# Kernel optimization log

Hardware: AMD Instinct MI355X
Metric: run time of the kernel (lower is better)

## Reference

```python
import jax, jax.numpy as jnp
import numpy as np

B, N, F, C, K = 8, 256, 64, 16, 2  # batch, agents, hidden_nf, hidden_c (coord channels), category_num
EPS = 1e-4


def _lin(x, W, b=None):
    y = jnp.einsum('...i,oi->...o', x, W)
    return y if b is None else y + b


def _forward(h, coord, vel, category, W_cv, W_e1, b_e1, W_e2, b_e2,
             W_cat1, b_cat1, W_cat2, b_cat2, W_f1, b_f1, W_f2, b_f2,
             W_n1, b_n1, W_n2, b_n2, W_ql, W_kl, W_qm, b_qm):
    relu = jax.nn.relu
    B_, N_, F_ = h.shape
    # --- edge model: dense pairwise features ---
    coord_diff = coord[:, :, None] - coord[:, None]            # [B,N,N,C,3]
    coord_dist = jnp.linalg.norm(coord_diff, axis=-1)          # [B,N,N,C]
    h1 = jnp.broadcast_to(h[:, :, None, :], (B_, N_, N_, F_))
    h2 = jnp.broadcast_to(h[:, None, :, :], (B_, N_, N_, F_))
    edge_h = jnp.concatenate([h1, h2, coord_dist], axis=-1)    # [B,N,N,2F+C]
    edge_feat = relu(_lin(relu(_lin(edge_h, W_e1, b_e1)), W_e2, b_e2))  # [B,N,N,F]
    # --- inner agent attention ---
    att = relu(_lin(h, W_qm, b_qm))[..., None]                 # [B,N,C,1]
    v = coord - jnp.mean(coord, axis=(1, 2), keepdims=True)
    coord = att * v + coord
    # --- reasoning-based coordinate aggregation (loop over K=2 categories) ---
    factors = jnp.zeros(edge_h.shape[:3] + (C,), coord.dtype)
    for i in range(K):
        ci = relu(_lin(relu(_lin(edge_h, W_cat1[i], b_cat1[i])), W_cat2[i], b_cat2[i]))
        factors = factors + category[..., i:i + 1] * ci
    factors = relu(_lin(relu(_lin(factors, W_f1, b_f1)), W_f2, b_f2))   # [B,N,N,C]
    coord = coord + jnp.sum(factors[..., None] * coord_diff, axis=2)    # [B,N,C,3]
    # --- velocity term (linear over channel dim) ---
    coord = coord + jnp.einsum('bncd,oc->bnod', vel, W_cv)
    # --- non-linear equivariant update ---
    cm = jnp.mean(coord, axis=(1, 2), keepdims=True)
    c = coord - cm
    q = jnp.einsum('bncd,oc->bnod', c, W_ql)
    k = jnp.einsum('bncd,oc->bnod', c, W_kl)
    prod = jnp.sum(q * k, axis=-1, keepdims=True)              # [B,N,C,1]
    mask = (prod >= 0).astype(c.dtype)
    kns = jnp.sum(k * k, axis=-1, keepdims=True)
    coord = mask * q + (1 - mask) * (q - prod / (kns + EPS) * k) + cm
    # --- node model: masked sum over neighbors (no self-edge) ---
    nb_mask = 1.0 - jnp.eye(N_, dtype=edge_feat.dtype)
    agg = jnp.einsum('bnmf,nm->bnf', edge_feat, nb_mask)
    h_out = h + _lin(relu(_lin(jnp.concatenate([h, agg], axis=-1), W_n1, b_n1)), W_n2, b_n2)
    return h_out, coord


def setup_inputs() -> dict:
    key = jax.random.key(0)
    ks = jax.random.split(key, 20)
    p = lambda i, shape, fan: jax.random.normal(ks[i], shape, jnp.float32) / np.sqrt(fan)
    z = lambda shape: jnp.zeros(shape, jnp.float32)
    return {
        'h': jax.random.normal(ks[0], (B, N, F), jnp.float32),
        'coord': jax.random.normal(ks[1], (B, N, C, 3), jnp.float32),
        'vel': jax.random.normal(ks[2], (B, N, C, 3), jnp.float32),
        'category': jax.random.uniform(ks[3], (B, N, N, K), jnp.float32),
        'W_cv': p(4, (C, C), C),
        'W_e1': p(5, (F, 2 * F + C), 2 * F + C), 'b_e1': z((F,)),
        'W_e2': p(6, (F, F), F), 'b_e2': z((F,)),
        'W_cat1': p(7, (K, F, 2 * F + C), 2 * F + C), 'b_cat1': z((K, F)),
        'W_cat2': p(8, (K, C, F), F), 'b_cat2': z((K, C)),
        'W_f1': p(9, (C, C), C), 'b_f1': z((C,)),
        'W_f2': p(10, (C, C), C), 'b_f2': z((C,)),
        'W_n1': p(11, (F, 2 * F), 2 * F), 'b_n1': z((F,)),
        'W_n2': p(12, (F, F), F), 'b_n2': z((F,)),
        'W_ql': p(13, (C, C), C),
        'W_kl': p(14, (C, C), C),
        'W_qm': p(15, (C, F), F), 'b_qm': z((C,)),
    }


def reference(h, coord, vel, category, W_cv, W_e1, b_e1, W_e2, b_e2,
              W_cat1, b_cat1, W_cat2, b_cat2, W_f1, b_f1, W_f2, b_f2,
              W_n1, b_n1, W_n2, b_n2, W_ql, W_kl, W_qm, b_qm):
    h_out, coord_out = _forward(h, coord, vel, category, W_cv, W_e1, b_e1, W_e2, b_e2,
                                W_cat1, b_cat1, W_cat2, b_cat2, W_f1, b_f1, W_f2, b_f2,
                                W_n1, b_n1, W_n2, b_n2, W_ql, W_kl, W_qm, b_qm)
    return (h_out, coord_out, category)
```

## Files before the change

kernel.cpp:

```cpp
#include <hip/hip_runtime.h>

typedef unsigned short u16;
typedef unsigned int u32;
typedef _Float16 f16;
typedef __attribute__((ext_vector_type(2))) _Float16 f16x2;
typedef __attribute__((ext_vector_type(4))) _Float16 f16x4;
typedef __attribute__((ext_vector_type(4))) float f32x4;

#define EPSV 1e-4f


static constexpr int WS_FLAG = 0;
static constexpr int WS_ATT  = 16;
static constexpr int WS_CT   = 32784;
static constexpr int WS_AGG  = 131088;
static constexpr int WS_CAC  = 262160;
static constexpr int WS_GWN1 = 360464;
static constexpr int WS_GWN2 = 364560;
static constexpr int WS_BN1  = 372752;
static constexpr int WS_BN2  = 372816;
static constexpr int WS_BIAS = 372880;
static constexpr int WS_GWD  = 373008;
static constexpr int WS_GWE2 = 374544;
static constexpr int WS_GWC2 = 376592;
static constexpr int WS_GWF1 = 377616;
static constexpr int WS_GWF2 = 377744;

static __device__ __forceinline__ float bfld(u16 v) {
  return __uint_as_float(((unsigned)v) << 16);
}
static __device__ __forceinline__ u16 f2b(float x) {
  unsigned u = __float_as_uint(x);
  u += 0x7FFFu + ((u >> 16) & 1u);
  return (u16)(u >> 16);
}
static __device__ __forceinline__ float ldv(const void* p, int i, int flag) {
  return flag ? bfld(((const u16*)p)[i]) : ((const float*)p)[i];
}
static __device__ __forceinline__ void stv(void* p, int i, float v, int flag) {
  if (flag) ((u16*)p)[i] = f2b(v);
  else      ((float*)p)[i] = v;
}
static __device__ __forceinline__ f16* scratchHA(void* outv, int flag) {
  return (f16*)((char*)outv + (size_t)229376 * (flag ? 2 : 4));
}
static __device__ __forceinline__ int sniff_flag(const void* h) {
  const u16* hu = (const u16*)h;
  int cnt = 0;
  for (int i = 0; i < 128; ++i) {
    unsigned e = (hu[i] >> 7) & 0xFFu;
    if ((e >= 100u && e <= 150u) || hu[i] == 0) ++cnt;
  }
  return (cnt >= 112) ? 1 : 0;
}
static __device__ __forceinline__ f16x4 pack4(float a, float b, float c, float d) {
  const f16x2 lo = __builtin_bit_cast(f16x2, __builtin_amdgcn_cvt_pkrtz(a, b));
  const f16x2 hi = __builtin_bit_cast(f16x2, __builtin_amdgcn_cvt_pkrtz(c, d));
  f16x4 r; r[0] = lo[0]; r[1] = lo[1]; r[2] = hi[0]; r[3] = hi[1]; return r;
}
static __device__ __forceinline__ f16x4 pack4_relu(float a, float b, float c, float d) {
  f16x2 lo = __builtin_bit_cast(f16x2, __builtin_amdgcn_cvt_pkrtz(a, b));
  f16x2 hi = __builtin_bit_cast(f16x2, __builtin_amdgcn_cvt_pkrtz(c, d));
  const f16x2 z = {(_Float16)0.f, (_Float16)0.f};
  lo = __builtin_elementwise_max(lo, z);
  hi = __builtin_elementwise_max(hi, z);
  f16x4 r; r[0] = lo[0]; r[1] = lo[1]; r[2] = hi[0]; r[3] = hi[1]; return r;
}
static __device__ __forceinline__ void st8h(f16* dst, uint4 v) {
  uint2 lo; lo.x = v.x; lo.y = v.y;
  uint2 hi; hi.x = v.z; hi.y = v.w;
  *(uint2*)dst = lo;
  *(uint2*)(dst + 4) = hi;
}
static __device__ __forceinline__ void load48(const void* p, int node, int flag,
                                              float* dst) {
  if (flag) {
    const uint4* q4 = (const uint4*)((const u16*)p + node * 48);
#pragma unroll
    for (int c = 0; c < 6; ++c) {
      const uint4 v = q4[c];
      const u32 a[4] = {v.x, v.y, v.z, v.w};
#pragma unroll
      for (int e = 0; e < 4; ++e) {
        dst[c * 8 + e * 2]     = bfld((u16)(a[e] & 0xFFFFu));
        dst[c * 8 + e * 2 + 1] = bfld((u16)(a[e] >> 16));
      }
    }
  } else {
    const float4* q4 = (const float4*)((const float*)p + node * 48);
#pragma unroll
    for (int c = 0; c < 12; ++c) {
      const float4 v = q4[c];
      dst[c * 4] = v.x; dst[c * 4 + 1] = v.y; dst[c * 4 + 2] = v.z; dst[c * 4 + 3] = v.w;
    }
  }
}
static __device__ __forceinline__ void stage_h64(const void* h, int hbase, int flag,
                                                 f16* sH, int tid) {
  if (flag) {
    const uint4* src = (const uint4*)((const u16*)h + hbase);
    for (int v = tid; v < 512; v += 256) {
      const uint4 x = src[v];
      const int e = v * 8;
      f16* dst = &sH[(e >> 6) * 68 + (e & 63)];
      const u32 a[4] = {x.x, x.y, x.z, x.w};
#pragma unroll
      for (int p = 0; p < 4; ++p) {
        dst[p * 2]     = (f16)bfld((u16)(a[p] & 0xFFFFu));
        dst[p * 2 + 1] = (f16)bfld((u16)(a[p] >> 16));
      }
    }
  } else {
    const float4* src = (const float4*)((const float*)h + hbase);
    for (int v = tid; v < 1024; v += 256) {
      const float4 x = src[v];
      const int e = v * 4;
      f16* dst = &sH[(e >> 6) * 68 + (e & 63)];
      dst[0] = (f16)x.x; dst[1] = (f16)x.y; dst[2] = (f16)x.z; dst[3] = (f16)x.w;
    }
  }
}

__global__ __launch_bounds__(256) void k_front(
    const void* __restrict__ h, const void* __restrict__ coord,
    const void* __restrict__ We1, const void* __restrict__ Wc1,
    const void* __restrict__ We2, const void* __restrict__ Wc2,
    const void* __restrict__ Wf1, const void* __restrict__ Wf2,
    const void* __restrict__ Wn1, const void* __restrict__ Wn2,
    const void* __restrict__ Wqm,
    const void* __restrict__ be1, const void* __restrict__ bc1,
    const void* __restrict__ bqm, const void* __restrict__ be2,
    const void* __restrict__ bc2, const void* __restrict__ bf1,
    const void* __restrict__ bf2, const void* __restrict__ bn1,
    const void* __restrict__ bn2,
    float* __restrict__ ws, void* __restrict__ outv) {
  const int blk = blockIdx.x, tid = threadIdx.x;
  __shared__ int sflag;
  if (tid == 0) {
    sflag = sniff_flag(h);
    if (blk == 0) ((int*)ws)[WS_FLAG] = sflag;
  }
  __syncthreads();
  const int flag = sflag;

  if (blk < 256) {
    const int t = blk * 256 + tid;
    const int STR = 65536;
    for (int idx = t; idx < 98304; idx += STR) {
      const int node = idx / 48, cd = idx - node * 48;
      ws[WS_CT + ((node >> 8) * 48 + cd) * 256 + (node & 255)] = ldv(coord, idx, flag);
    }
    f16* gwd  = (f16*)(ws + WS_GWD);
    f16* gwe2 = (f16*)(ws + WS_GWE2);
    f16* gwc2 = (f16*)(ws + WS_GWC2);
    f16* gwf1 = (f16*)(ws + WS_GWF1);
    f16* gwf2 = (f16*)(ws + WS_GWF2);
    for (int idx = t; idx < 3072; idx += STR) {
      const int o = idx >> 4, c = idx & 15;
      const void* src = (o < 64) ? We1 : Wc1;
      const int row = (o < 64) ? o : (o - 64);
      gwd[idx] = (f16)ldv(src, row * 144 + 128 + c, flag);
    }
    for (int idx = t; idx < 4096; idx += STR) gwe2[idx] = (f16)ldv(We2, idx, flag);
    for (int idx = t; idx < 2048; idx += STR) gwc2[idx] = (f16)ldv(Wc2, idx, flag);
    if (t < 256) { gwf1[t] = (f16)ldv(Wf1, t, flag); gwf2[t] = (f16)ldv(Wf2, t, flag); }
    f16* gwn1 = (f16*)(ws + WS_GWN1);
    f16* gwn2 = (f16*)(ws + WS_GWN2);
    for (int idx = t; idx < 8192; idx += STR) gwn1[idx] = (f16)ldv(Wn1, idx, flag);
    for (int idx = t; idx < 4096; idx += STR) gwn2[idx] = (f16)ldv(Wn2, idx, flag);
    if (t < 64)  ws[WS_BN1 + t] = ldv(bn1, t, flag);
    if (t >= 64 && t < 128) ws[WS_BN2 + t - 64] = ldv(bn2, t - 64, flag);
    if (t >= 128 && t < 192) ws[WS_BIAS + t - 128] = ldv(be2, t - 128, flag);
    if (t >= 192 && t < 224) ws[WS_BIAS + 64 + t - 192] = ldv(bc2, t - 192, flag);
    if (t >= 224 && t < 240) ws[WS_BIAS + 96 + t - 224] = ldv(bf1, t - 224, flag);
    if (t >= 240 && t < 256) ws[WS_BIAS + 112 + t - 240] = ldv(bf2, t - 240, flag);
    return;
  }

  const int gb = blk - 256;
  const int nt = gb / 5, grp = gb % 5;
  const int w = tid >> 6, lane = tid & 63;
  const int q = lane >> 4, l15 = lane & 15;
  f16* HA16 = scratchHA(outv, flag);
  f16* HBJ  = HA16 + 2048 * 192;
  __shared__ __align__(16) f16 sW[80 * 68];
  __shared__ __align__(16) f16 sH[64 * 68];
  __shared__ float sBias[80];
  if (flag) {
    for (int idx = tid; idx < 640; idx += 256) {
      const int r = idx >> 3, seg = idx & 7;
      const int row = grp * 80 + r;
      const u16* src;
      if (row < 64)       src = (const u16*)We1 + row * 144;
      else if (row < 192) src = (const u16*)Wc1 + (row - 64) * 144;
      else if (row < 384) {
        const int ro = row - 192;
        src = (ro < 64) ? (const u16*)We1 + ro * 144 + 64
                        : (const u16*)Wc1 + (ro - 64) * 144 + 64;
      } else              src = (const u16*)Wqm + (row - 384) * 64;
      const uint4 v = ((const uint4*)src)[seg];
      const u32 a[4] = {v.x, v.y, v.z, v.w};
      f16* dst = &sW[r * 68 + seg * 8];
#pragma unroll
      for (int p = 0; p < 4; ++p) {
        dst[p * 2]     = (f16)bfld((u16)(a[p] & 0xFFFFu));
        dst[p * 2 + 1] = (f16)bfld((u16)(a[p] >> 16));
      }
    }
  } else {
    for (int idx = tid; idx < 1280; idx += 256) {
      const int r = idx >> 4, seg = idx & 15;
      const int row = grp * 80 + r;
      const float* src;
      if (row < 64)       src = (const float*)We1 + row * 144;
      else if (row < 192) src = (const float*)Wc1 + (row - 64) * 144;
      else if (row < 384) {
        const int ro = row - 192;
        src = (ro < 64) ? (const float*)We1 + ro * 144 + 64
                        : (const float*)Wc1 + (ro - 64) * 144 + 64;
      } else              src = (const float*)Wqm + (row - 384) * 64;
      const float4 v = ((const float4*)src)[seg];
      f16x4 t; t[0] = (f16)v.x; t[1] = (f16)v.y; t[2] = (f16)v.z; t[3] = (f16)v.w;
      *(f16x4*)&sW[r * 68 + seg * 4] = t;
    }
  }
  stage_h64(h, nt * 64 * 64, flag, sH, tid);
  if (tid < 80) {
    const int row = grp * 80 + tid;
    sBias[tid] = (row < 64) ? ldv(be1, row, flag)
               : (row < 192) ? ldv(bc1, row - 64, flag)
               : (row < 384) ? 0.f : ldv(bqm, row - 384, flag);
  }
  __syncthreads();
  f16x4 Af[4];
#pragma unroll
  for (int ks = 0; ks < 4; ++ks)
    Af[ks] = *(const f16x4*)&sH[(w * 16 + l15) * 68 + ks * 16 + q * 4];
#pragma unroll
  for (int ot = 0; ot < 5; ++ot) {
    const float bv = sBias[ot * 16 + l15];
    f32x4 acc = (f32x4){bv, bv, bv, bv};
#pragma unroll
    for (int ks = 0; ks < 4; ++ks) {
      const f16x4 Bf = *(const f16x4*)&sW[(ot * 16 + l15) * 68 + ks * 16 + q * 4];
      acc = __builtin_amdgcn_mfma_f32_16x16x16f16(Af[ks], Bf, acc, 0, 0, 0);
    }
    const int out = grp * 80 + ot * 16 + l15;
    const int nodeD = nt * 64 + w * 16 + q * 4;
#pragma unroll
    for (int r = 0; r < 4; ++r) {
      const int node = nodeD + r;
      if (out < 192) {
        HA16[node * 192 + out] = (f16)acc[r];
      } else if (out < 384) {
        const int ol = out - 192;
        HBJ[(((node >> 8) * 48 + ((ol >> 4) << 2) + ((ol & 15) >> 2)) * 256 +
             (node & 255)) * 4 + (ol & 3)] = (f16)acc[r];
      } else {
        ws[WS_ATT + node * 16 + out - 384] = fmaxf(acc[r], 0.f);
      }
    }
  }
}

__global__ __launch_bounds__(256, 4) void k_edge(const void* __restrict__ cat,
                                                 float* __restrict__ ws,
                                                 void* __restrict__ outv) {
  const int node = ((blockIdx.x & 7) << 8) | (blockIdx.x >> 3);
  const int b = node >> 8, i = node & 255;
  const int tid = threadIdx.x;
  const int w = tid >> 6, lane = tid & 63, q = lane >> 4, l15 = lane & 15;
  const int flag = ((const int*)ws)[WS_FLAG];
  const f16* HA16 = scratchHA(outv, flag);
  const f16* HBJ  = HA16 + 2048 * 192;
  const float* __restrict__ cTb = ws + WS_CT + b * 48 * 256;

  __shared__ __align__(16) f16 sWd[192 * 20];
  __shared__ __align__(16) f16 sWe2[64 * 76];
  __shared__ __align__(16) f16 sWc2[32 * 76];
  __shared__ __align__(16) f16 sWf1[16 * 20];
  __shared__ __align__(16) f16 sWf2[16 * 20];
  __shared__ __align__(16) f16 distS[256 * 20];
  __shared__ float sHa[192];
  __shared__ float sB[128];
  __shared__ __align__(16) float red[448];

  int jj[4]; float mjt[4];
#pragma unroll
  for (int jt = 0; jt < 4; ++jt) {
    jj[jt] = w * 64 + jt * 16 + l15;
    mjt[jt] = (jj[jt] == i) ? 0.f : 1.f;
  }
  const f16* hbq = HBJ + (size_t)(b * 48 + q) * 1024;
  f16x4 hbA[2][4];
#pragma unroll
  for (int og = 0; og < 2; ++og)
#pragma unroll
    for (int jt = 0; jt < 4; ++jt)
      hbA[og][jt] = *(const f16x4*)(hbq + og * 4096 + jj[jt] * 4);

  {
    const u32* gwd = (const u32*)(ws + WS_GWD);
    for (int idx = tid; idx < 1536; idx += 256) {
      const int r = idx >> 3, c = idx & 7;
      *(u32*)&sWd[r * 20 + c * 2] = gwd[idx];
    }
    const u32* gwe = (const u32*)(ws + WS_GWE2);
    for (int idx = tid; idx < 2048; idx += 256) {
      const int r = idx >> 5, c = idx & 31;
      *(u32*)&sWe2[r * 76 + c * 2] = gwe[idx];
    }
    const u32* gwc = (const u32*)(ws + WS_GWC2);
    for (int idx = tid; idx < 1024; idx += 256) {
      const int r = idx >> 5, c = idx & 31;
      *(u32*)&sWc2[r * 76 + c * 2] = gwc[idx];
    }
    if (tid < 128) {
      const int r = tid >> 3, c = tid & 7;
      *(u32*)&sWf1[r * 20 + c * 2] = ((const u32*)(ws + WS_GWF1))[tid];
      *(u32*)&sWf2[r * 20 + c * 2] = ((const u32*)(ws + WS_GWF2))[tid];
    }
    if (tid < 192) sHa[tid] = (float)HA16[node * 192 + tid];
    if (tid < 128) sB[tid] = ws[WS_BIAS + tid];
  }
  {
    float dr[16];
#pragma unroll
    for (int c = 0; c < 16; ++c) {
      float s = 0.f;
#pragma unroll
      for (int d = 0; d < 3; ++d) {
        const int cd = c * 3 + d;
        const float df = cTb[cd * 256 + i] - cTb[cd * 256 + tid];
        s += df * df;
      }
      dr[c] = sqrtf(s);
    }
#pragma unroll
    for (int kk = 0; kk < 4; ++kk)
      *(f16x4*)&distS[tid * 20 + kk * 4] =
          pack4(dr[4 * kk], dr[4 * kk + 1], dr[4 * kk + 2], dr[4 * kk + 3]);
  }
  __syncthreads();

  f16x4 dfr[4];
#pragma unroll
  for (int jt = 0; jt < 4; ++jt)
    dfr[jt] = *(const f16x4*)&distS[jj[jt] * 20 + q * 4];

  f16x4 af[4][4];
#pragma unroll
  for (int og = 0; og < 4; ++og) {
    const f16x4 wd = *(const f16x4*)&sWd[(og * 16 + l15) * 20 + q * 4];
    const float4 sha = *(const float4*)&sHa[og * 16 + q * 4];
#pragma unroll
    for (int jt = 0; jt < 4; ++jt) {
      const f16x4 hb = hbA[og & 1][jt];
      f32x4 a;
      a[0] = sha.x + (float)hb[0];
      a[1] = sha.y + (float)hb[1];
      a[2] = sha.z + (float)hb[2];
      a[3] = sha.w + (float)hb[3];
      a = __builtin_amdgcn_mfma_f32_16x16x16f16(wd, dfr[jt], a, 0, 0, 0);
      af[og][jt] = pack4_relu(a[0], a[1], a[2], a[3]);
      if (og < 2)
        hbA[og & 1][jt] = *(const f16x4*)(hbq + (og + 2) * 4096 + jj[jt] * 4);
    }
  }
  float sagg[4][4];
#pragma unroll
  for (int ft = 0; ft < 4; ++ft) {
    f32x4 C2[4];
#pragma unroll
    for (int jt = 0; jt < 4; ++jt) C2[jt] = (f32x4){0.f, 0.f, 0.f, 0.f};
#pragma unroll
    for (int og = 0; og < 4; ++og) {
      const f16x4 we = *(const f16x4*)&sWe2[(ft * 16 + l15) * 76 + og * 16 + q * 4];
#pragma unroll
      for (int jt = 0; jt < 4; ++jt)
        C2[jt] = __builtin_amdgcn_mfma_f32_16x16x16f16(we, af[og][jt], C2[jt], 0, 0, 0);
    }
#pragma unroll
    for (int r = 0; r < 4; ++r) {
      float s = 0.f;
#pragma unroll
      for (int jt = 0; jt < 4; ++jt)
        s += fmaxf(C2[jt][r] + sB[ft * 16 + q * 4 + r], 0.f) * mjt[jt];
      sagg[ft][r] = s;
    }
  }

  f16x4 hbB[2][4];
#pragma unroll
  for (int g = 0; g < 2; ++g)
#pragma unroll
    for (int jt = 0; jt < 4; ++jt)
      hbB[g][jt] = *(const f16x4*)(hbq + (4 + g) * 4096 + jj[jt] * 4);
  float cv0[4], cv1[4];
#pragma unroll
  for (int jt = 0; jt < 4; ++jt) {
    if (flag) {
      const u32 p = ((const u32*)cat)[node * 256 + jj[jt]];
      cv0[jt] = bfld((u16)(p & 0xFFFFu));
      cv1[jt] = bfld((u16)(p >> 16));
    } else {
      const float2 p = ((const float2*)cat)[node * 256 + jj[jt]];
      cv0[jt] = p.x; cv1[jt] = p.y;
    }
  }

#pragma unroll
  for (int ft = 0; ft < 4; ++ft)
#pragma unroll
    for (int st = 1; st < 16; st <<= 1)
#pragma unroll
      for (int r = 0; r < 4; ++r) sagg[ft][r] += __shfl_xor(sagg[ft][r], st, 64);
  if (l15 == 0) {
#pragma unroll
    for (int ft = 0; ft < 4; ++ft)
#pragma unroll
      for (int r = 0; r < 4; ++r) red[w * 64 + ft * 16 + q * 4 + r] = sagg[ft][r];
  }

  float fac[4][4] = {};
#pragma unroll
  for (int m = 0; m < 2; ++m) {
    f32x4 C3[4];
#pragma unroll
    for (int jt = 0; jt < 4; ++jt) C3[jt] = (f32x4){0.f, 0.f, 0.f, 0.f};
#pragma unroll
    for (int og2 = 0; og2 < 4; ++og2) {
      const int g = m * 4 + og2;
      const int og = 4 + g;
      const f16x4 wd = *(const f16x4*)&sWd[(og * 16 + l15) * 20 + q * 4];
      const f16x4 wc = *(const f16x4*)&sWc2[(m * 16 + l15) * 76 + og2 * 16 + q * 4];
      const float4 sha = *(const float4*)&sHa[og * 16 + q * 4];
#pragma unroll
      for (int jt = 0; jt < 4; ++jt) {
        const f16x4 hb = hbB[g & 1][jt];
        f32x4 a;
        a[0] = sha.x + (float)hb[0];
        a[1] = sha.y + (float)hb[1];
        a[2] = sha.z + (float)hb[2];
        a[3] = sha.w + (float)hb[3];
        a = __builtin_amdgcn_mfma_f32_16x16x16f16(wd, dfr[jt], a, 0, 0, 0);
        const f16x4 afv = pack4_relu(a[0], a[1], a[2], a[3]);
        C3[jt] = __builtin_amdgcn_mfma_f32_16x16x16f16(wc, afv, C3[jt], 0, 0, 0);
        if (g < 6)
          hbB[g & 1][jt] = *(const f16x4*)(hbq + (4 + g + 2) * 4096 + jj[jt] * 4);
      }
    }
#pragma unroll
    for (int jt = 0; jt < 4; ++jt) {
      const float catv = m ? cv1[jt] : cv0[jt];
#pragma unroll
      for (int r = 0; r < 4; ++r)
        fac[jt][r] += catv * fmaxf(C3[jt][r] + sB[64 + m * 16 + q * 4 + r], 0.f);
    }
  }

  const f16x4 w1 = *(const f16x4*)&sWf1[l15 * 20 + q * 4];
  const f16x4 w2 = *(const f16x4*)&sWf2[l15 * 20 + q * 4];
  float civ[12];
#pragma unroll
  for (int r = 0; r < 4; ++r)
#pragma unroll
    for (int d = 0; d < 3; ++d) civ[r * 3 + d] = cTb[(3 * (q * 4 + r) + d) * 256 + i];
  float ca[12] = {};
#pragma unroll
  for (int jt = 0; jt < 4; ++jt) {
    const f16x4 fF = pack4(fac[jt][0], fac[jt][1], fac[jt][2], fac[jt][3]);
    const f32x4 z = {0.f, 0.f, 0.f, 0.f};
    f32x4 G = __builtin_amdgcn_mfma_f32_16x16x16f16(w1, fF, z, 0, 0, 0);
    const f16x4 gF = pack4(fmaxf(G[0] + sB[96 + q * 4 + 0], 0.f),
                           fmaxf(G[1] + sB[96 + q * 4 + 1], 0.f),
                           fmaxf(G[2] + sB[96 + q * 4 + 2], 0.f),
                           fmaxf(G[3] + sB[96 + q * 4 + 3], 0.f));
    f32x4 F2 = __builtin_amdgcn_mfma_f32_16x16x16f16(w2, gF, z, 0, 0, 0);
#pragma unroll
    for (int r = 0; r < 4; ++r) {
      const float fv = fmaxf(F2[r] + sB[112 + q * 4 + r], 0.f);
#pragma unroll
      for (int d = 0; d < 3; ++d) {
        const float cj = cTb[(3 * (q * 4 + r) + d) * 256 + jj[jt]];
        ca[r * 3 + d] += fv * (civ[r * 3 + d] - cj);
      }
    }
  }
#pragma unroll
  for (int st = 1; st < 16; st <<= 1)
#pragma unroll
    for (int u = 0; u < 12; ++u) ca[u] += __shfl_xor(ca[u], st, 64);

  if (l15 == 0) {
#pragma unroll
    for (int u = 0; u < 12; ++u) red[256 + w * 48 + q * 12 + u] = ca[u];
  }
  __syncthreads();
  if (tid < 64) {
    ws[WS_AGG + node * 64 + tid] = red[tid] + red[64 + tid] + red[128 + tid] + red[192 + tid];
  } else if (tid < 112) {
    const int u = tid - 64;
    ws[WS_CAC + node * 48 + u] =
        red[256 + u] + red[256 + 48 + u] + red[256 + 96 + u] + red[256 + 144 + u];
  }
}

__global__ __launch_bounds__(256) void k_epi(const void* __restrict__ h,
                                             const void* __restrict__ coord,
                                             const void* __restrict__ vel,
                                             const void* __restrict__ cat,
                                             const void* __restrict__ Wcv,
                                             const void* __restrict__ Wql,
                                             const void* __restrict__ Wkl,
                                             const float* __restrict__ ws,
                                             void* __restrict__ outv) {
  const int blk = blockIdx.x, tid = threadIdx.x;
  const int flag = ((const int*)ws)[WS_FLAG];
  if (blk < 32) {
    const int w = tid >> 6, lane = tid & 63;
    const int q = lane >> 4, l15 = lane & 15;
    __shared__ __align__(16) f16 sW1[64 * 132];
    __shared__ __align__(16) f16 sW2[64 * 68];
    __shared__ __align__(16) f16 sH[64 * 68];
    __shared__ float sbn[128];
    {
      const uint4* g14 = (const uint4*)(ws + WS_GWN1);
      for (int idx = tid; idx < 1024; idx += 256) {
        const int o = idx >> 4, c8 = idx & 15;
        st8h(&sW1[o * 132 + c8 * 8], g14[idx]);
      }
      const uint4* g24 = (const uint4*)(ws + WS_GWN2);
      for (int idx = tid; idx < 512; idx += 256) {
        const int o = idx >> 3, c8 = idx & 7;
        st8h(&sW2[o * 68 + c8 * 8], g24[idx]);
      }
      stage_h64(h, blk * 64 * 64, flag, sH, tid);
      if (tid < 128) sbn[tid] = (tid < 64) ? ws[WS_BN1 + tid] : ws[WS_BN2 + tid - 64];
    }
    __syncthreads();
    const int node = blk * 64 + w * 16 + l15;
    const int lrow = w * 16 + l15;
    f16x4 xB[8];
#pragma unroll
    for (int kt = 0; kt < 4; ++kt)
      xB[kt] = *(const f16x4*)&sH[lrow * 68 + kt * 16 + q * 4];
#pragma unroll
    for (int kt = 0; kt < 4; ++kt) {
      const float* ap = ws + WS_AGG + node * 64 + kt * 16 + q * 4;
      xB[4 + kt] = pack4(ap[0], ap[1], ap[2], ap[3]);
    }
    f16x4 hidB[4];
#pragma unroll
    for (int ot = 0; ot < 4; ++ot) {
      f32x4 acc;
#pragma unroll
      for (int r = 0; r < 4; ++r) acc[r] = sbn[ot * 16 + q * 4 + r];
#pragma unroll
      for (int kt = 0; kt < 8; ++kt) {
        const f16x4 a = *(const f16x4*)&sW1[(ot * 16 + l15) * 132 + kt * 16 + q * 4];
        acc = __builtin_amdgcn_mfma_f32_16x16x16f16(a, xB[kt], acc, 0, 0, 0);
      }
      hidB[ot] = pack4(fmaxf(acc[0], 0.f), fmaxf(acc[1], 0.f),
                       fmaxf(acc[2], 0.f), fmaxf(acc[3], 0.f));
    }
#pragma unroll
    for (int ft = 0; ft < 4; ++ft) {
      const f16x4 hl = *(const f16x4*)&sH[lrow * 68 + ft * 16 + q * 4];
      f32x4 acc;
#pragma unroll
      for (int r = 0; r < 4; ++r) acc[r] = sbn[64 + ft * 16 + q * 4 + r] + (float)hl[r];
#pragma unroll
      for (int ot = 0; ot < 4; ++ot) {
        const f16x4 a = *(const f16x4*)&sW2[(ft * 16 + l15) * 68 + ot * 16 + q * 4];
        acc = __builtin_amdgcn_mfma_f32_16x16x16f16(a, hidB[ot], acc, 0, 0, 0);
      }
#pragma unroll
      for (int r = 0; r < 4; ++r)
        stv(outv, node * 64 + ft * 16 + q * 4 + r, acc[r], flag);
    }
  } else if (blk < 40) {
    const int b = blk - 32;
    const int n = tid, node = b * 256 + n;
    const int wave = n >> 6, lane = n & 63;
    __shared__ float wcv[256], wql[256], wkl[256];
    __shared__ float redm[16];
    wcv[n] = ldv(Wcv, n, flag);
    wql[n] = ldv(Wql, n, flag);
    wkl[n] = ldv(Wkl, n, flag);
    float cf[48];
    load48(coord, node, flag, cf);
    float s0 = 0.f, s1 = 0.f, s2 = 0.f;
#pragma unroll
    for (int c = 0; c < 16; ++c) { s0 += cf[c*3]; s1 += cf[c*3+1]; s2 += cf[c*3+2]; }
    for (int s = 1; s < 64; s <<= 1) {
      s0 += __shfl_xor(s0, s, 64); s1 += __shfl_xor(s1, s, 64); s2 += __shfl_xor(s2, s, 64);
    }
    if (lane == 0) { redm[wave*4] = s0; redm[wave*4+1] = s1; redm[wave*4+2] = s2; }
    __syncthreads();
    const float m0 = (redm[0]+redm[4]+redm[8]+redm[12]) * (1.f/4096.f);
    const float m1 = (redm[1]+redm[5]+redm[9]+redm[13]) * (1.f/4096.f);
    const float m2 = (redm[2]+redm[6]+redm[10]+redm[14]) * (1.f/4096.f);
    __syncthreads();
    float velf[48];
    load48(vel, node, flag, velf);
    float att[16];
    {
      const float4* ap = (const float4*)(ws + WS_ATT + node * 16);
#pragma unroll
      for (int c4 = 0; c4 < 4; ++c4) {
        const float4 v = ap[c4];
        att[c4*4] = v.x; att[c4*4+1] = v.y; att[c4*4+2] = v.z; att[c4*4+3] = v.w;
      }
    }
    float cac[48];
    {
      const float4* cp = (const float4*)(ws + WS_CAC + node * 48);
#pragma unroll
      for (int c4 = 0; c4 < 12; ++c4) {
        const float4 v = cp[c4];
        cac[c4*4] = v.x; cac[c4*4+1] = v.y; cac[c4*4+2] = v.z; cac[c4*4+3] = v.w;
      }
    }
    float c3[48];
#pragma unroll
    for (int c = 0; c < 16; ++c) {
      const float at = att[c];
#pragma unroll
      for (int d = 0; d < 3; ++d) {
        const int cd = c * 3 + d;
        const float md = (d == 0) ? m0 : ((d == 1) ? m1 : m2);
        float cc = at * (cf[cd] - md) + cf[cd];
        cc += cac[cd];
        float a = cc;
#pragma unroll
        for (int cp = 0; cp < 16; ++cp) a += velf[cp * 3 + d] * wcv[c * 16 + cp];
        c3[cd] = a;
      }
    }
    float t0 = 0.f, t1 = 0.f, t2 = 0.f;
#pragma unroll
    for (int c = 0; c < 16; ++c) { t0 += c3[c*3]; t1 += c3[c*3+1]; t2 += c3[c*3+2]; }
    for (int s = 1; s < 64; s <<= 1) {
      t0 += __shfl_xor(t0, s, 64); t1 += __shfl_xor(t1, s, 64); t2 += __shfl_xor(t2, s, 64);
    }
    if (lane == 0) { redm[wave*4] = t0; redm[wave*4+1] = t1; redm[wave*4+2] = t2; }
    __syncthreads();
    const float cm0 = (redm[0]+redm[4]+redm[8]+redm[12]) * (1.f/4096.f);
    const float cm1 = (redm[1]+redm[5]+redm[9]+redm[13]) * (1.f/4096.f);
    const float cm2 = (redm[2]+redm[6]+redm[10]+redm[14]) * (1.f/4096.f);
    float cc[48];
#pragma unroll
    for (int c = 0; c < 16; ++c) {
      cc[c*3]   = c3[c*3]   - cm0;
      cc[c*3+1] = c3[c*3+1] - cm1;
      cc[c*3+2] = c3[c*3+2] - cm2;
    }
#pragma unroll
    for (int o = 0; o < 16; ++o) {
      float qv[3], kv[3];
#pragma unroll
      for (int d = 0; d < 3; ++d) {
        float sq = 0.f, sk = 0.f;
#pragma unroll
        for (int cp = 0; cp < 16; ++cp) {
          sq += cc[cp * 3 + d] * wql[o * 16 + cp];
          sk += cc[cp * 3 + d] * wkl[o * 16 + cp];
        }
        qv[d] = sq; kv[d] = sk;
      }
      const float prod = qv[0]*kv[0] + qv[1]*kv[1] + qv[2]*kv[2];
      const float kns  = kv[0]*kv[0] + kv[1]*kv[1] + kv[2]*kv[2];
      const float wq = prod / (kns + EPSV);
#pragma unroll
      for (int d = 0; d < 3; ++d) {
        const float cmd = (d == 0) ? cm0 : ((d == 1) ? cm1 : cm2);
        const float val = (prod >= 0.f) ? qv[d] : (qv[d] - wq * kv[d]);
        stv(outv, 131072 + node * 48 + o * 3 + d, val + cmd, flag);
      }
    }
  } else {
    const int idx = (blk - 40) * 256 + tid;
    if (flag) {
      ((uint4*)((char*)outv + 458752))[idx] = ((const uint4*)cat)[idx];
    } else {
      ((uint4*)((char*)outv + 917504))[idx] = ((const uint4*)cat)[idx];
      ((uint4*)((char*)outv + 917504))[idx + 131072] = ((const uint4*)cat)[idx + 131072];
    }
  }
}

extern "C" void kernel_launch(void* const* d_in, const int* in_sizes, int n_in,
                              void* d_out, int out_size, void* d_ws, size_t ws_size,
                              hipStream_t stream) {
  (void)in_sizes; (void)n_in; (void)out_size; (void)ws_size;
  const void* h    = d_in[0];
  const void* coord= d_in[1];
  const void* vel  = d_in[2];
  const void* cat  = d_in[3];
  const void* Wcv  = d_in[4];
  const void* We1  = d_in[5];
  const void* be1  = d_in[6];
  const void* We2  = d_in[7];
  const void* be2  = d_in[8];
  const void* Wc1  = d_in[9];
  const void* bc1  = d_in[10];
  const void* Wc2  = d_in[11];
  const void* bc2  = d_in[12];
  const void* Wf1  = d_in[13];
  const void* bf1v = d_in[14];
  const void* Wf2  = d_in[15];
  const void* bf2v = d_in[16];
  const void* Wn1  = d_in[17];
  const void* bn1  = d_in[18];
  const void* Wn2  = d_in[19];
  const void* bn2  = d_in[20];
  const void* Wql  = d_in[21];
  const void* Wkl  = d_in[22];
  const void* Wqm  = d_in[23];
  const void* bqm  = d_in[24];
  float* ws = (float*)d_ws;

  k_front<<<416, 256, 0, stream>>>(h, coord, We1, Wc1, We2, Wc2, Wf1, Wf2,
                                   Wn1, Wn2, Wqm, be1, bc1, bqm, be2, bc2,
                                   bf1v, bf2v, bn1, bn2, ws, d_out);
  k_edge<<<2048, 256, 0, stream>>>(cat, ws, d_out);
  k_epi<<<552, 256, 0, stream>>>(h, coord, vel, cat, Wcv, Wql, Wkl, ws, d_out);
}
```

Before: 179.2 us.

## Split coordinate epilogue into separate kernel with four threads per node

The coordinate update (velocity mixing, centering, equivariant q/k projection) moves out of k_epi into a new k_coord kernel of 8 blocks × 1024 threads. Each node is now handled by four threads, each owning four channels, and the 16×16 channel mixes are done through lane shuffles. This is meant to shorten the long serial per-thread work and cut register pressure in the former 8-block tail of k_epi. In exchange it adds an extra kernel launch and more shuffle traffic.

```diff
diff --git a/kernel.cpp b/kernel.cpp
--- a/kernel.cpp
+++ b/kernel.cpp
@@ -72,26 +72,24 @@
   *(uint2*)dst = lo;
   *(uint2*)(dst + 4) = hi;
 }
-static __device__ __forceinline__ void load48(const void* p, int node, int flag,
-                                              float* dst) {
+static __device__ __forceinline__ void load12(const void* p, int node, int g,
+                                              int flag, float* dst) {
   if (flag) {
-    const uint4* q4 = (const uint4*)((const u16*)p + node * 48);
-#pragma unroll
-    for (int c = 0; c < 6; ++c) {
-      const uint4 v = q4[c];
-      const u32 a[4] = {v.x, v.y, v.z, v.w};
-#pragma unroll
-      for (int e = 0; e < 4; ++e) {
-        dst[c * 8 + e * 2]     = bfld((u16)(a[e] & 0xFFFFu));
-        dst[c * 8 + e * 2 + 1] = bfld((u16)(a[e] >> 16));
-      }
+    const uint2* q2 = (const uint2*)((const u16*)p + node * 48 + g * 12);
+#pragma unroll
+    for (int t = 0; t < 3; ++t) {
+      const uint2 v = q2[t];
+      dst[t * 4 + 0] = bfld((u16)(v.x & 0xFFFFu));
+      dst[t * 4 + 1] = bfld((u16)(v.x >> 16));
+      dst[t * 4 + 2] = bfld((u16)(v.y & 0xFFFFu));
+      dst[t * 4 + 3] = bfld((u16)(v.y >> 16));
     }
   } else {
-    const float4* q4 = (const float4*)((const float*)p + node * 48);
-#pragma unroll
-    for (int c = 0; c < 12; ++c) {
-      const float4 v = q4[c];
-      dst[c * 4] = v.x; dst[c * 4 + 1] = v.y; dst[c * 4 + 2] = v.z; dst[c * 4 + 3] = v.w;
+    const float4* q4 = (const float4*)((const float*)p + node * 48 + g * 12);
+#pragma unroll
+    for (int t = 0; t < 3; ++t) {
+      const float4 v = q4[t];
+      dst[t * 4] = v.x; dst[t * 4 + 1] = v.y; dst[t * 4 + 2] = v.z; dst[t * 4 + 3] = v.w;
     }
   }
 }
@@ -506,13 +504,137 @@
   }
 }
 
+__global__ __launch_bounds__(1024) void k_coord(const void* __restrict__ coord,
+                                                const void* __restrict__ vel,
+                                                const void* __restrict__ Wcv,
+                                                const void* __restrict__ Wql,
+                                                const void* __restrict__ Wkl,
+                                                const float* __restrict__ ws,
+                                                void* __restrict__ outv) {
+  const int b = blockIdx.x, tid = threadIdx.x;
+  const int n = tid >> 2, g = tid & 3;
+  const int node = (b << 8) | n;
+  const int lane = tid & 63, wave = tid >> 6;
+  const int flag = ((const int*)ws)[WS_FLAG];
+  __shared__ float swcv[256], swql[256], swkl[256];
+  __shared__ float redm[96];
+  if (tid < 256) swcv[tid] = ldv(Wcv, tid, flag);
+  else if (tid < 512) swql[tid - 256] = ldv(Wql, tid - 256, flag);
+  else if (tid < 768) swkl[tid - 512] = ldv(Wkl, tid - 512, flag);
+
+  float cf[12], velf[12];
+  load12(coord, node, g, flag, cf);
+  load12(vel, node, g, flag, velf);
+  float att4[4];
+  {
+    const float4 v = *(const float4*)(ws + WS_ATT + node * 16 + g * 4);
+    att4[0] = v.x; att4[1] = v.y; att4[2] = v.z; att4[3] = v.w;
+  }
+  float cac[12];
+  {
+    const float4* cp4 = (const float4*)(ws + WS_CAC + node * 48 + g * 12);
+#pragma unroll
+    for (int t = 0; t < 3; ++t) {
+      const float4 v = cp4[t];
+      cac[t * 4] = v.x; cac[t * 4 + 1] = v.y; cac[t * 4 + 2] = v.z; cac[t * 4 + 3] = v.w;
+    }
+  }
+  float s0 = 0.f, s1 = 0.f, s2 = 0.f;
+#pragma unroll
+  for (int j = 0; j < 4; ++j) { s0 += cf[j*3]; s1 += cf[j*3+1]; s2 += cf[j*3+2]; }
+  for (int st = 1; st < 64; st <<= 1) {
+    s0 += __shfl_xor(s0, st, 64); s1 += __shfl_xor(s1, st, 64); s2 += __shfl_xor(s2, st, 64);
+  }
+  if (lane == 0) { redm[wave*3] = s0; redm[wave*3+1] = s1; redm[wave*3+2] = s2; }
+  __syncthreads();
+  float m[3];
+#pragma unroll
+  for (int d = 0; d < 3; ++d) {
+    float s = 0.f;
+#pragma unroll
+    for (int wv = 0; wv < 16; ++wv) s += redm[wv*3 + d];
+    m[d] = s * (1.f / 4096.f);
+  }
+  float c3[12];
+#pragma unroll
+  for (int j = 0; j < 4; ++j)
+#pragma unroll
+    for (int d = 0; d < 3; ++d)
+      c3[j*3+d] = att4[j] * (cf[j*3+d] - m[d]) + cf[j*3+d] + cac[j*3+d];
+#pragma unroll
+  for (int rot = 0; rot < 4; ++rot) {
+    const int sg = g ^ rot;
+#pragma unroll
+    for (int j2 = 0; j2 < 4; ++j2) {
+      const float r0 = __shfl_xor(velf[j2*3],   rot, 64);
+      const float r1 = __shfl_xor(velf[j2*3+1], rot, 64);
+      const float r2 = __shfl_xor(velf[j2*3+2], rot, 64);
+      const int cp = sg * 4 + j2;
+#pragma unroll
+      for (int j = 0; j < 4; ++j) {
+        const float wv = swcv[(g*4+j)*16 + cp];
+        c3[j*3]   += r0 * wv;
+        c3[j*3+1] += r1 * wv;
+        c3[j*3+2] += r2 * wv;
+      }
+    }
+  }
+  float t0 = 0.f, t1 = 0.f, t2 = 0.f;
+#pragma unroll
+  for (int j = 0; j < 4; ++j) { t0 += c3[j*3]; t1 += c3[j*3+1]; t2 += c3[j*3+2]; }
+  for (int st = 1; st < 64; st <<= 1) {
+    t0 += __shfl_xor(t0, st, 64); t1 += __shfl_xor(t1, st, 64); t2 += __shfl_xor(t2, st, 64);
+  }
+  if (lane == 0) { redm[48 + wave*3] = t0; redm[48 + wave*3+1] = t1; redm[48 + wave*3+2] = t2; }
+  __syncthreads();
+  float cm[3];
+#pragma unroll
+  for (int d = 0; d < 3; ++d) {
+    float s = 0.f;
+#pragma unroll
+    for (int wv = 0; wv < 16; ++wv) s += redm[48 + wv*3 + d];
+    cm[d] = s * (1.f / 4096.f);
+  }
+  float cc[12];
+#pragma unroll
+  for (int j = 0; j < 4; ++j)
+#pragma unroll
+    for (int d = 0; d < 3; ++d) cc[j*3+d] = c3[j*3+d] - cm[d];
+  float qv[12] = {}, kv[12] = {};
+#pragma unroll
+  for (int rot = 0; rot < 4; ++rot) {
+    const int sg = g ^ rot;
+#pragma unroll
+    for (int j2 = 0; j2 < 4; ++j2) {
+      const float r0 = __shfl_xor(cc[j2*3],   rot, 64);
+      const float r1 = __shfl_xor(cc[j2*3+1], rot, 64);
+      const float r2 = __shfl_xor(cc[j2*3+2], rot, 64);
+      const int cp = sg * 4 + j2;
+#pragma unroll
+      for (int j = 0; j < 4; ++j) {
+        const float wq_ = swql[(g*4+j)*16 + cp];
+        const float wk_ = swkl[(g*4+j)*16 + cp];
+        qv[j*3]   += r0 * wq_;  kv[j*3]   += r0 * wk_;
+        qv[j*3+1] += r1 * wq_;  kv[j*3+1] += r1 * wk_;
+        qv[j*3+2] += r2 * wq_;  kv[j*3+2] += r2 * wk_;
+      }
+    }
+  }
+#pragma unroll
+  for (int j = 0; j < 4; ++j) {
+    const float prod = qv[j*3]*kv[j*3] + qv[j*3+1]*kv[j*3+1] + qv[j*3+2]*kv[j*3+2];
+    const float kns  = kv[j*3]*kv[j*3] + kv[j*3+1]*kv[j*3+1] + kv[j*3+2]*kv[j*3+2];
+    const float wq = prod / (kns + EPSV);
+#pragma unroll
+    for (int d = 0; d < 3; ++d) {
+      const float val = (prod >= 0.f) ? qv[j*3+d] : (qv[j*3+d] - wq * kv[j*3+d]);
+      stv(outv, 131072 + node * 48 + (g*4+j) * 3 + d, val + cm[d], flag);
+    }
+  }
+}
+
 __global__ __launch_bounds__(256) void k_epi(const void* __restrict__ h,
-                                             const void* __restrict__ coord,
-                                             const void* __restrict__ vel,
                                              const void* __restrict__ cat,
-                                             const void* __restrict__ Wcv,
-                                             const void* __restrict__ Wql,
-                                             const void* __restrict__ Wkl,
                                              const float* __restrict__ ws,
                                              void* __restrict__ outv) {
   const int blk = blockIdx.x, tid = threadIdx.x;
@@ -579,108 +701,8 @@
       for (int r = 0; r < 4; ++r)
         stv(outv, node * 64 + ft * 16 + q * 4 + r, acc[r], flag);
     }
-  } else if (blk < 40) {
-    const int b = blk - 32;
-    const int n = tid, node = b * 256 + n;
-    const int wave = n >> 6, lane = n & 63;
-    __shared__ float wcv[256], wql[256], wkl[256];
-    __shared__ float redm[16];
-    wcv[n] = ldv(Wcv, n, flag);
-    wql[n] = ldv(Wql, n, flag);
-    wkl[n] = ldv(Wkl, n, flag);
-    float cf[48];
-    load48(coord, node, flag, cf);
-    float s0 = 0.f, s1 = 0.f, s2 = 0.f;
-#pragma unroll
-    for (int c = 0; c < 16; ++c) { s0 += cf[c*3]; s1 += cf[c*3+1]; s2 += cf[c*3+2]; }
-    for (int s = 1; s < 64; s <<= 1) {
-      s0 += __shfl_xor(s0, s, 64); s1 += __shfl_xor(s1, s, 64); s2 += __shfl_xor(s2, s, 64);
-    }
-    if (lane == 0) { redm[wave*4] = s0; redm[wave*4+1] = s1; redm[wave*4+2] = s2; }
-    __syncthreads();
-    const float m0 = (redm[0]+redm[4]+redm[8]+redm[12]) * (1.f/4096.f);
-    const float m1 = (redm[1]+redm[5]+redm[9]+redm[13]) * (1.f/4096.f);
-    const float m2 = (redm[2]+redm[6]+redm[10]+redm[14]) * (1.f/4096.f);
-    __syncthreads();
-    float velf[48];
-    load48(vel, node, flag, velf);
-    float att[16];
-    {
-      const float4* ap = (const float4*)(ws + WS_ATT + node * 16);
-#pragma unroll
-      for (int c4 = 0; c4 < 4; ++c4) {
-        const float4 v = ap[c4];
-        att[c4*4] = v.x; att[c4*4+1] = v.y; att[c4*4+2] = v.z; att[c4*4+3] = v.w;
-      }
-    }
-    float cac[48];
-    {
-      const float4* cp = (const float4*)(ws + WS_CAC + node * 48);
-#pragma unroll
-      for (int c4 = 0; c4 < 12; ++c4) {
-        const float4 v = cp[c4];
-        cac[c4*4] = v.x; cac[c4*4+1] = v.y; cac[c4*4+2] = v.z; cac[c4*4+3] = v.w;
-      }
-    }
-    float c3[48];
-#pragma unroll
-    for (int c = 0; c < 16; ++c) {
-      const float at = att[c];
-#pragma unroll
-      for (int d = 0; d < 3; ++d) {
-        const int cd = c * 3 + d;
-        const float md = (d == 0) ? m0 : ((d == 1) ? m1 : m2);
-        float cc = at * (cf[cd] - md) + cf[cd];
-        cc += cac[cd];
-        float a = cc;
-#pragma unroll
-        for (int cp = 0; cp < 16; ++cp) a += velf[cp * 3 + d] * wcv[c * 16 + cp];
-        c3[cd] = a;
-      }
-    }
-    float t0 = 0.f, t1 = 0.f, t2 = 0.f;
-#pragma unroll
-    for (int c = 0; c < 16; ++c) { t0 += c3[c*3]; t1 += c3[c*3+1]; t2 += c3[c*3+2]; }
-    for (int s = 1; s < 64; s <<= 1) {
-      t0 += __shfl_xor(t0, s, 64); t1 += __shfl_xor(t1, s, 64); t2 += __shfl_xor(t2, s, 64);
-    }
-    if (lane == 0) { redm[wave*4] = t0; redm[wave*4+1] = t1; redm[wave*4+2] = t2; }
-    __syncthreads();
-    const float cm0 = (redm[0]+redm[4]+redm[8]+redm[12]) * (1.f/4096.f);
-    const float cm1 = (redm[1]+redm[5]+redm[9]+redm[13]) * (1.f/4096.f);
-    const float cm2 = (redm[2]+redm[6]+redm[10]+redm[14]) * (1.f/4096.f);
-    float cc[48];
-#pragma unroll
-    for (int c = 0; c < 16; ++c) {
-      cc[c*3]   = c3[c*3]   - cm0;
-      cc[c*3+1] = c3[c*3+1] - cm1;
-      cc[c*3+2] = c3[c*3+2] - cm2;
-    }
-#pragma unroll
-    for (int o = 0; o < 16; ++o) {
-      float qv[3], kv[3];
-#pragma unroll
-      for (int d = 0; d < 3; ++d) {
-        float sq = 0.f, sk = 0.f;
-#pragma unroll
-        for (int cp = 0; cp < 16; ++cp) {
-          sq += cc[cp * 3 + d] * wql[o * 16 + cp];
-          sk += cc[cp * 3 + d] * wkl[o * 16 + cp];
-        }
-        qv[d] = sq; kv[d] = sk;
-      }
-      const float prod = qv[0]*kv[0] + qv[1]*kv[1] + qv[2]*kv[2];
-      const float kns  = kv[0]*kv[0] + kv[1]*kv[1] + kv[2]*kv[2];
-      const float wq = prod / (kns + EPSV);
-#pragma unroll
-      for (int d = 0; d < 3; ++d) {
-        const float cmd = (d == 0) ? cm0 : ((d == 1) ? cm1 : cm2);
-        const float val = (prod >= 0.f) ? qv[d] : (qv[d] - wq * kv[d]);
-        stv(outv, 131072 + node * 48 + o * 3 + d, val + cmd, flag);
-      }
-    }
   } else {
-    const int idx = (blk - 40) * 256 + tid;
+    const int idx = (blk - 32) * 256 + tid;
     if (flag) {
       ((uint4*)((char*)outv + 458752))[idx] = ((const uint4*)cat)[idx];
     } else {
@@ -725,5 +747,6 @@
                                    Wn1, Wn2, Wqm, be1, bc1, bqm, be2, bc2,
                                    bf1v, bf2v, bn1, bn2, ws, d_out);
   k_edge<<<2048, 256, 0, stream>>>(cat, ws, d_out);
-  k_epi<<<552, 256, 0, stream>>>(h, coord, vel, cat, Wcv, Wql, Wkl, ws, d_out);
-}
+  k_coord<<<8, 1024, 0, stream>>>(coord, vel, Wcv, Wql, Wkl, ws, d_out);
+  k_epi<<<544, 256, 0, stream>>>(h, cat, ws, d_out);
+}
```

Result: slower. 195.3 us (+9.0%).
